# Kernel tuning notes

Measured on AMD Instinct MI355X. Metric: run time of the kernel, lower is better.

Reference implementation:

```python
import jax, jax.numpy as jnp
import numpy as np

N_NODES = 50000


def gcn_conv(x, W, b, src, dst, n_nodes):
    """PyG-style GCNConv: out = D^{-1/2} (A + I) D^{-1/2} (x W) + b."""
    xw = x @ W  # [N, out_dim]
    loop = jnp.arange(n_nodes, dtype=src.dtype)
    src_f = jnp.concatenate([src, loop])  # edges + self-loops
    dst_f = jnp.concatenate([dst, loop])
    deg = jax.ops.segment_sum(jnp.ones_like(dst_f, dtype=xw.dtype), dst_f,
                              num_segments=n_nodes)
    dinv = jnp.where(deg > 0, jax.lax.rsqrt(deg), 0.0)
    norm = dinv[src_f] * dinv[dst_f]  # [E+N]
    msgs = xw[src_f] * norm[:, None]  # gather + scale
    out = jax.ops.segment_sum(msgs, dst_f, num_segments=n_nodes)
    return out + b


def setup_inputs() -> dict:
    key = jax.random.key(0)
    ks = jax.random.split(key, 8)
    n, e = N_NODES, 800000
    in_d, hid, out_d = 128, 256, 64
    x = jax.random.normal(ks[0], (n, in_d), dtype=jnp.float32)
    edge_index = jax.random.randint(ks[1], (2, e), 0, n, dtype=jnp.int32)
    sc = lambda f: 1.0 / np.sqrt(f)
    W1 = jax.random.normal(ks[2], (in_d, hid), dtype=jnp.float32) * sc(in_d)
    b1 = jnp.zeros((hid,), jnp.float32)
    W2 = jax.random.normal(ks[3], (hid, hid), dtype=jnp.float32) * sc(hid)
    b2 = jnp.zeros((hid,), jnp.float32)
    W_final = jax.random.normal(ks[4], (hid, out_d), dtype=jnp.float32) * sc(hid)
    b_final = jnp.zeros((out_d,), jnp.float32)
    W_skip = jax.random.normal(ks[5], (in_d, out_d), dtype=jnp.float32) * sc(in_d)
    b_skip = jnp.zeros((out_d,), jnp.float32)
    return {"x": x, "edge_index": edge_index, "W1": W1, "b1": b1,
            "W2": W2, "b2": b2, "W_final": W_final, "b_final": b_final,
            "W_skip": W_skip, "b_skip": b_skip}


def reference(x, edge_index, W1, b1, W2, b2, W_final, b_final, W_skip, b_skip):
    n = x.shape[0]
    src, dst = edge_index[0], edge_index[1]
    h = jax.nn.relu(gcn_conv(x, W1, b1, src, dst, n))
    h = jax.nn.relu(gcn_conv(h, W2, b2, src, dst, n))
    return h @ W_final + b_final + (x @ W_skip + b_skip)
```

## Files before the change

### kernel.cpp

```cpp
#include <hip/hip_runtime.h>

#define N_NODES 50000
#define N_EDGES 800000
#define HB 782

typedef float f32x4 __attribute__((ext_vector_type(4)));
typedef float f32x2 __attribute__((ext_vector_type(2)));
typedef __bf16 bf16x8 __attribute__((ext_vector_type(8)));
typedef __bf16 bf16x4 __attribute__((ext_vector_type(4)));


__global__ void zero_deg(int4* __restrict__ p, int n4) {
    int i = blockIdx.x * blockDim.x + threadIdx.x;
    if (i < n4) p[i] = make_int4(0, 0, 0, 0);
}

#define CAST_N4 (N_NODES * 32)
#define PREP_ITEMS (CAST_N4 + 32768 + 65536 + 16384 + 8192 + 64)
#define PREP_BLOCKS ((PREP_ITEMS + 255) / 256)

__global__ void mega_prep(const int* __restrict__ dst, int* __restrict__ deg,
                          int* __restrict__ rank,
                          const float* __restrict__ x, __bf16* __restrict__ x_bf,
                          const float* __restrict__ W1, const float* __restrict__ W2,
                          const float* __restrict__ Wf, const float* __restrict__ Ws,
                          const float* __restrict__ bfb, const float* __restrict__ bsb,
                          __bf16* __restrict__ W1t, __bf16* __restrict__ W2t,
                          __bf16* __restrict__ Wft, __bf16* __restrict__ Wst,
                          float* __restrict__ bfinal) {
    int b = blockIdx.x;
    if (b < HB) {
        int i = (b * 256 + threadIdx.x) * 4;
        if (i >= N_EDGES) return;
        int4 d = *(const int4*)(dst + i);
        int4 r;
        r.x = atomicAdd(&deg[d.x], 1);
        r.y = atomicAdd(&deg[d.y], 1);
        r.z = atomicAdd(&deg[d.z], 1);
        r.w = atomicAdd(&deg[d.w], 1);
        *(int4*)(rank + i) = r;
        return;
    }
    int idx = (b - HB) * 256 + threadIdx.x;
    if (idx < CAST_N4) {
        float4 v = ((const float4*)x)[idx];
        bf16x4 a = {(__bf16)v.x, (__bf16)v.y, (__bf16)v.z, (__bf16)v.w};
        __builtin_nontemporal_store(a, (bf16x4*)x_bf + idx);
        return;
    }
    int j = idx - CAST_N4;
    if (j < 32768) {
        int n = j >> 7, k = j & 127;
        W1t[j] = (__bf16)W1[k * 256 + n];
    } else if (j < 32768 + 65536) {
        int i = j - 32768;
        int n = i >> 8, k = i & 255;
        W2t[i] = (__bf16)W2[k * 256 + n];
    } else if (j < 32768 + 65536 + 16384) {
        int i = j - (32768 + 65536);
        int n = i >> 8, k = i & 255;
        Wft[i] = (__bf16)Wf[k * 64 + n];
    } else if (j < 32768 + 65536 + 16384 + 8192) {
        int i = j - (32768 + 65536 + 16384);
        int n = i >> 7, k = i & 127;
        Wst[i] = (__bf16)Ws[k * 64 + n];
    } else if (j < 32768 + 65536 + 16384 + 8192 + 64) {
        int i = j - (32768 + 65536 + 16384 + 8192);
        bfinal[i] = bfb[i] + bsb[i];
    }
}

__device__ __forceinline__ int wave_incl_scan(int x) {
    int lane = threadIdx.x & 63;
#pragma unroll
    for (int off = 1; off < 64; off <<= 1) {
        int y = __shfl_up(x, off, 64);
        if (lane >= off) x += y;
    }
    return x;
}

__global__ void scan_partial_dinv(const int* __restrict__ in, int n,
                                  int* __restrict__ out_partial, int* __restrict__ blocksum,
                                  float* __restrict__ dinv) {
    __shared__ int wsum[8];
    int i = blockIdx.x * 512 + threadIdx.x;
    int v = (i < n) ? in[i] : 0;
    if (i < n) dinv[i] = rsqrtf((float)(v + 1));
    int inc = wave_incl_scan(v);
    int lane = threadIdx.x & 63, wid = threadIdx.x >> 6;
    if (lane == 63) wsum[wid] = inc;
    __syncthreads();
    if (wid == 0) {
        int w = (lane < 8) ? wsum[lane] : 0;
        int wi = wave_incl_scan(w);
        if (lane < 8) wsum[lane] = wi;
    }
    __syncthreads();
    int woff = (wid == 0) ? 0 : wsum[wid - 1];
    if (i < n) out_partial[i] = woff + inc - v;
    if (threadIdx.x == 0) blocksum[blockIdx.x] = wsum[7];
}

#define SCAN_NB 98
#define XS_ITEMS (N_NODES * 16)
#define XS_BLOCKS ((XS_ITEMS + 511) / 512)

__global__ __launch_bounds__(512) void scan_add_xs(int* __restrict__ rowptr, int n,
                                                   const int* __restrict__ blocksum, int nb, int total,
                                                   const __bf16* __restrict__ x_bf,
                                                   const float* __restrict__ dinv,
                                                   unsigned char* __restrict__ x_s8) {
    int b = blockIdx.x;
    if (b < SCAN_NB) {
        __shared__ int sexc[128];
        __shared__ int w0tot;
        int t = threadIdx.x;
        if (t < 128) {
            int v = (t < nb) ? blocksum[t] : 0;
            int inc = wave_incl_scan(v);
            sexc[t] = inc - v;
            if (t == 63) w0tot = inc;
        }
        __syncthreads();
        int boff = sexc[b] + (b >= 64 ? w0tot : 0);
        int i = b * 512 + t;
        if (i < n) rowptr[i] += boff;
        if (i == 0) rowptr[n] = total;
        return;
    }
    int j = (b - SCAN_NB) * 512 + threadIdx.x;
    if (j < XS_ITEMS) {
        bf16x8 v = ((const bf16x8*)x_bf)[j];
        float di = dinv[j >> 4];
        float f[8];
#pragma unroll
        for (int k = 0; k < 8; ++k) f[k] = di * (float)v[k];
        int w0 = __builtin_amdgcn_cvt_pk_fp8_f32(f[0], f[1], 0, false);
        w0 = __builtin_amdgcn_cvt_pk_fp8_f32(f[2], f[3], w0, true);
        int w1 = __builtin_amdgcn_cvt_pk_fp8_f32(f[4], f[5], 0, false);
        w1 = __builtin_amdgcn_cvt_pk_fp8_f32(f[6], f[7], w1, true);
        ((uint2*)x_s8)[j] = make_uint2((unsigned)w0, (unsigned)w1);
    }
}

__global__ void fill_csr(const int* __restrict__ src, const int* __restrict__ dst,
                         const int* __restrict__ rank,
                         const int* __restrict__ rowptr, int* __restrict__ csr_src) {
    int i = (blockIdx.x * blockDim.x + threadIdx.x) * 4;
    if (i >= N_EDGES) return;
    int4 d = *(const int4*)(dst + i);
    int4 s = *(const int4*)(src + i);
    int4 r = *(const int4*)(rank + i);
    csr_src[rowptr[d.x] + r.x] = s.x;
    csr_src[rowptr[d.y] + r.y] = s.y;
    csr_src[rowptr[d.z] + r.z] = s.z;
    csr_src[rowptr[d.w] + r.w] = s.w;
}


template <int F> struct LdSel;
template <> struct LdSel<128> { using T = unsigned int; };
template <> struct LdSel<256> { using T = uint2; };

template <int F>
__global__ __launch_bounds__(256) void aggregate_fp8(const unsigned char* __restrict__ in_s, __bf16* __restrict__ out,
                                                     const int* __restrict__ rowptr, const int* __restrict__ csr_src,
                                                     const float* __restrict__ dinv) {
    constexpr int BPL = F / 32;
    using LT = typename LdSel<F>::T;
    int node = blockIdx.x * 4 + (threadIdx.x >> 6);
    int lane = threadIdx.x & 63;
    int lh = lane & 31;
    int half = lane >> 5;
    const unsigned char* colbase = in_s + lh * BPL;

    float acc[BPL] = {};
    auto decode_acc = [&](LT v) {
        if constexpr (BPL == 4) {
            f32x2 p0 = __builtin_amdgcn_cvt_pk_f32_fp8(v, false);
            f32x2 p1 = __builtin_amdgcn_cvt_pk_f32_fp8(v, true);
            acc[0] += p0[0]; acc[1] += p0[1]; acc[2] += p1[0]; acc[3] += p1[1];
        } else {
            f32x2 p0 = __builtin_amdgcn_cvt_pk_f32_fp8(v.x, false);
            f32x2 p1 = __builtin_amdgcn_cvt_pk_f32_fp8(v.x, true);
            f32x2 p2 = __builtin_amdgcn_cvt_pk_f32_fp8(v.y, false);
            f32x2 p3 = __builtin_amdgcn_cvt_pk_f32_fp8(v.y, true);
            acc[0] += p0[0]; acc[1] += p0[1]; acc[2] += p1[0]; acc[3] += p1[1];
            acc[4] += p2[0]; acc[5] += p2[1]; acc[6] += p3[0]; acc[7] += p3[1];
        }
    };

    if (half == 0) decode_acc(*(const LT*)(colbase + (size_t)node * F));

    int beg = rowptr[node], end = rowptr[node + 1];
    int e = beg;
    for (; e + 16 <= end; e += 16) {
        int ss[8];
#pragma unroll
        for (int k = 0; k < 8; ++k) ss[k] = csr_src[e + 2 * k + half];
        LT v[8];
#pragma unroll
        for (int k = 0; k < 8; ++k) v[k] = *(const LT*)(colbase + (size_t)ss[k] * F);
#pragma unroll
        for (int k = 0; k < 8; ++k) decode_acc(v[k]);
    }
    for (; e + 8 <= end; e += 8) {
        int s0 = csr_src[e + half], s1 = csr_src[e + 2 + half];
        int s2 = csr_src[e + 4 + half], s3 = csr_src[e + 6 + half];
        LT v0 = *(const LT*)(colbase + (size_t)s0 * F);
        LT v1 = *(const LT*)(colbase + (size_t)s1 * F);
        LT v2 = *(const LT*)(colbase + (size_t)s2 * F);
        LT v3 = *(const LT*)(colbase + (size_t)s3 * F);
        decode_acc(v0); decode_acc(v1); decode_acc(v2); decode_acc(v3);
    }
    for (; e + 2 <= end; e += 2) {
        int s = csr_src[e + half];
        decode_acc(*(const LT*)(colbase + (size_t)s * F));
    }
    if (e < end && half == 0) decode_acc(*(const LT*)(colbase + (size_t)csr_src[e] * F));

    float di = dinv[node];
    if constexpr (BPL == 4) {
        bf16x4 o;
#pragma unroll
        for (int j = 0; j < 4; ++j) {
            float t = acc[j] + __shfl_xor(acc[j], 32);
            o[j] = (__bf16)(di * t);
        }
        if (half == 0) __builtin_nontemporal_store(o, (bf16x4*)(out + (size_t)node * F + lh * 4));
    } else {
        bf16x8 o;
#pragma unroll
        for (int j = 0; j < 8; ++j) {
            float t = acc[j] + __shfl_xor(acc[j], 32);
            o[j] = (__bf16)(di * t);
        }
        if (half == 0) __builtin_nontemporal_store(o, (bf16x8*)(out + (size_t)node * F + lh * 8));
    }
}


template <int NROWS, int NTH>
__device__ __forceinline__ void stage_tile(const __bf16* __restrict__ src, int K, int row0, int rowclamp,
                                           int k0, char* lds) {
    int t = threadIdx.x;
#pragma unroll
    for (int p = 0; p < NROWS * 8 / NTH; ++p) {
        int G = p * NTH + t;
        int r = G >> 3, gp = G & 7;
        int g = gp ^ (r & 7);
        int gr = row0 + r;
        if (gr > rowclamp) gr = rowclamp;
        const __bf16* sp = src + (size_t)gr * K + k0 + g * 8;
        __builtin_amdgcn_global_load_lds((const __attribute__((address_space(1))) void*)sp,
                                         (__attribute__((address_space(3))) void*)(lds + G * 16), 16, 0, 0);
    }
}


template <bool SCALE, bool OUT_FP8>
__global__ __launch_bounds__(512, 4) void mfma_gemm_wide(const __bf16* __restrict__ A, const __bf16* __restrict__ Bt,
                                                         int K, const float* __restrict__ bias,
                                                         const float* __restrict__ dinv,
                                                         void* __restrict__ Cout, int M) {
    constexpr int N = 256;
    __shared__ alignas(16) char lds[81920];
    const int lane = threadIdx.x & 63, wid = threadIdx.x >> 6;
    const int row0 = blockIdx.x * 64;
    const int kg = lane >> 4, l15 = lane & 15;

    f32x4 acc[4][2];
#pragma unroll
    for (int mi = 0; mi < 4; ++mi)
#pragma unroll
        for (int ni = 0; ni < 2; ++ni) acc[mi][ni] = {0.f, 0.f, 0.f, 0.f};

    auto STAGE = [&](int buf, int k0) {
        char* base = lds + buf * 40960;
        stage_tile<64, 512>(A, K, row0, M - 1, k0, base);
        stage_tile<256, 512>(Bt, K, 0, N - 1, k0, base + 8192);
    };

    const int nt = K >> 6;
    STAGE(0, 0);
    __syncthreads();
    int cur = 0;
    for (int t = 0; t < nt; ++t) {
        if (t + 1 < nt) STAGE(cur ^ 1, (t + 1) * 64);
        char* As = lds + cur * 40960;
        char* Bs = As + 8192;
        bf16x8 af[4][2], bfr[2][2];
#pragma unroll
        for (int mi = 0; mi < 4; ++mi) {
            int r = mi * 16 + l15;
#pragma unroll
            for (int kf = 0; kf < 2; ++kf) {
                int slot = (kf * 4 + kg) ^ (r & 7);
                af[mi][kf] = *(const bf16x8*)(As + r * 128 + slot * 16);
            }
        }
#pragma unroll
        for (int ni = 0; ni < 2; ++ni) {
            int r = wid * 32 + ni * 16 + l15;
#pragma unroll
            for (int kf = 0; kf < 2; ++kf) {
                int slot = (kf * 4 + kg) ^ (r & 7);
                bfr[ni][kf] = *(const bf16x8*)(Bs + r * 128 + slot * 16);
            }
        }
#pragma unroll
        for (int mi = 0; mi < 4; ++mi)
#pragma unroll
            for (int ni = 0; ni < 2; ++ni)
#pragma unroll
                for (int kf = 0; kf < 2; ++kf)
                    acc[mi][ni] = __builtin_amdgcn_mfma_f32_16x16x32_bf16(af[mi][kf], bfr[ni][kf],
                                                                          acc[mi][ni], 0, 0, 0);
        __syncthreads();
        cur ^= 1;
    }

#pragma unroll
    for (int mi = 0; mi < 4; ++mi) {
#pragma unroll
        for (int q = 0; q < 4; ++q) {
            int gr = row0 + mi * 16 + kg * 4 + q;
            if (gr >= M) continue;
            float sc = SCALE ? dinv[gr] : 1.0f;
            int col0 = wid * 32 + l15;
            float v0 = fmaxf(acc[mi][0][q] + bias[col0], 0.f);
            float v1 = fmaxf(acc[mi][1][q] + bias[col0 + 16], 0.f);
            if (SCALE) { v0 *= sc; v1 *= sc; }
            if constexpr (OUT_FP8) {
                int w = __builtin_amdgcn_cvt_pk_fp8_f32(v0, v1, 0, false);
                unsigned char* Cp = (unsigned char*)Cout + (size_t)gr * N;
                Cp[col0] = (unsigned char)(w & 0xff);
                Cp[col0 + 16] = (unsigned char)((w >> 8) & 0xff);
            } else {
                __bf16* Cp = (__bf16*)Cout + (size_t)gr * N;
                Cp[col0] = (__bf16)v0;
                Cp[col0 + 16] = (__bf16)v1;
            }
        }
    }
}


__global__ __launch_bounds__(256, 4) void mfma_gemm_final(const __bf16* __restrict__ A1, const __bf16* __restrict__ B1t, int K1,
                                                          const __bf16* __restrict__ A2, const __bf16* __restrict__ B2t, int K2,
                                                          const float* __restrict__ bias, float* __restrict__ Cout, int M) {
    constexpr int N = 64;
    __shared__ alignas(16) char lds[32768];
    const int lane = threadIdx.x & 63, wid = threadIdx.x >> 6;
    const int wm = wid >> 1, wn = wid & 1;
    const int row0 = blockIdx.x * 64;
    const int kg = lane >> 4, l15 = lane & 15;

    f32x4 acc[2][2];
#pragma unroll
    for (int mi = 0; mi < 2; ++mi)
#pragma unroll
        for (int ni = 0; ni < 2; ++ni) acc[mi][ni] = {0.f, 0.f, 0.f, 0.f};

    const int nt1 = K1 >> 6, nt = nt1 + (K2 >> 6);
    auto STAGE = [&](int buf, int tile) {
        const __bf16* A = (tile < nt1) ? A1 : A2;
        const __bf16* Bt = (tile < nt1) ? B1t : B2t;
        int K = (tile < nt1) ? K1 : K2;
        int k0 = ((tile < nt1) ? tile : tile - nt1) * 64;
        char* base = lds + buf * 16384;
        stage_tile<64, 256>(A, K, row0, M - 1, k0, base);
        stage_tile<64, 256>(Bt, K, 0, N - 1, k0, base + 8192);
    };

    STAGE(0, 0);
    __syncthreads();
    int cur = 0;
    for (int t = 0; t < nt; ++t) {
        if (t + 1 < nt) STAGE(cur ^ 1, t + 1);
        char* As = lds + cur * 16384;
        char* Bs = As + 8192;
        bf16x8 af[2][2], bfr[2][2];
#pragma unroll
        for (int mi = 0; mi < 2; ++mi) {
            int r = wm * 32 + mi * 16 + l15;
#pragma unroll
            for (int kf = 0; kf < 2; ++kf) {
                int slot = (kf * 4 + kg) ^ (r & 7);
                af[mi][kf] = *(const bf16x8*)(As + r * 128 + slot * 16);
            }
        }
#pragma unroll
        for (int ni = 0; ni < 2; ++ni) {
            int r = wn * 32 + ni * 16 + l15;
#pragma unroll
            for (int kf = 0; kf < 2; ++kf) {
                int slot = (kf * 4 + kg) ^ (r & 7);
                bfr[ni][kf] = *(const bf16x8*)(Bs + r * 128 + slot * 16);
            }
        }
#pragma unroll
        for (int mi = 0; mi < 2; ++mi)
#pragma unroll
            for (int ni = 0; ni < 2; ++ni)
#pragma unroll
                for (int kf = 0; kf < 2; ++kf)
                    acc[mi][ni] = __builtin_amdgcn_mfma_f32_16x16x32_bf16(af[mi][kf], bfr[ni][kf],
                                                                          acc[mi][ni], 0, 0, 0);
        __syncthreads();
        cur ^= 1;
    }

#pragma unroll
    for (int mi = 0; mi < 2; ++mi) {
#pragma unroll
        for (int ni = 0; ni < 2; ++ni) {
            int col = wn * 32 + ni * 16 + l15;
            float bv = bias[col];
#pragma unroll
            for (int q = 0; q < 4; ++q) {
                int gr = row0 + wm * 32 + mi * 16 + kg * 4 + q;
                if (gr < M) Cout[(size_t)gr * N + col] = acc[mi][ni][q] + bv;
            }
        }
    }
}


extern "C" void kernel_launch(void* const* d_in, const int* in_sizes, int n_in,
                              void* d_out, int out_size, void* d_ws, size_t ws_size,
                              hipStream_t stream) {
    const float* x  = (const float*)d_in[0];
    const int*   ei = (const int*)d_in[1];
    const int*   src = ei;
    const int*   dst = ei + N_EDGES;
    const float* W1 = (const float*)d_in[2];
    const float* b1 = (const float*)d_in[3];
    const float* W2 = (const float*)d_in[4];
    const float* b2 = (const float*)d_in[5];
    const float* Wf = (const float*)d_in[6];
    const float* bf = (const float*)d_in[7];
    const float* Ws = (const float*)d_in[8];
    const float* bs = (const float*)d_in[9];
    float* out = (float*)d_out;

    char* ws = (char*)d_ws;
    size_t off = 0;
    auto alloc = [&](size_t bytes) -> void* {
        void* p = ws + off;
        off += (bytes + 255) & ~(size_t)255;
        return p;
    };
    int*           deg      = (int*)alloc(N_NODES * 4);
    int*           rank     = (int*)alloc(N_EDGES * 4);
    int*           rowptr   = (int*)alloc((N_NODES + 1) * 4);
    float*         dinv     = (float*)alloc(N_NODES * 4);
    int*           blocksum = (int*)alloc(4096);
    int*           csr      = (int*)alloc(N_EDGES * 4);
    __bf16*        x_bf     = (__bf16*)alloc((size_t)N_NODES * 128 * 2);
    unsigned char* x_s8     = (unsigned char*)alloc((size_t)N_NODES * 128);
    __bf16*        W1t      = (__bf16*)alloc(128 * 256 * 2);
    __bf16*        W2t      = (__bf16*)alloc(256 * 256 * 2);
    __bf16*        Wft      = (__bf16*)alloc(256 * 64 * 2);
    __bf16*        Wst      = (__bf16*)alloc(128 * 64 * 2);
    float*         bfinal   = (float*)alloc(64 * 4);
    __bf16*        bufP1    = (__bf16*)alloc((size_t)N_NODES * 256 * 2);
    unsigned char* bufP2    = (unsigned char*)alloc((size_t)N_NODES * 256);
    __bf16*        bufP3    = (__bf16*)alloc((size_t)N_NODES * 256 * 2);

    zero_deg<<<(N_NODES / 4 + 255) / 256, 256, 0, stream>>>((int4*)deg, N_NODES / 4);

    mega_prep<<<HB + PREP_BLOCKS, 256, 0, stream>>>(dst, deg, rank, x, x_bf,
                                                    W1, W2, Wf, Ws, bf, bs,
                                                    W1t, W2t, Wft, Wst, bfinal);

    scan_partial_dinv<<<SCAN_NB, 512, 0, stream>>>(deg, N_NODES, rowptr, blocksum, dinv);

    scan_add_xs<<<SCAN_NB + XS_BLOCKS, 512, 0, stream>>>(rowptr, N_NODES, blocksum, SCAN_NB, N_EDGES,
                                                         x_bf, dinv, x_s8);

    fill_csr<<<HB, 256, 0, stream>>>(src, dst, rank, rowptr, csr);

    const int gm64 = (N_NODES + 63) / 64;

    aggregate_fp8<128><<<(N_NODES + 3) / 4, 256, 0, stream>>>(x_s8, bufP1, rowptr, csr, dinv);
    mfma_gemm_wide<true, true><<<gm64, 512, 0, stream>>>(bufP1, W1t, 128, b1, dinv, bufP2, N_NODES);

    aggregate_fp8<256><<<(N_NODES + 3) / 4, 256, 0, stream>>>(bufP2, bufP3, rowptr, csr, dinv);
    mfma_gemm_wide<false, false><<<gm64, 512, 0, stream>>>(bufP3, W2t, 256, b2, nullptr, bufP1, N_NODES);

    mfma_gemm_final<<<gm64, 256, 0, stream>>>(bufP1, Wft, 256, x_bf, Wst, 128, bfinal, out, N_NODES);
}
```

Baseline: 183.9 us.

## Compute skip GEMM alongside CSR fill and accumulate final GEMM into output

Moves the x@W_skip + bias skip-branch GEMM out of the final GEMM into extra blocks of the CSR fill kernel, so it runs concurrently with the memory-bound scatter. The final GEMM then only does the K=256 product and read-modify-writes into the output. This shortens the tail kernel's K loop but adds a read of the fp32 output in the last kernel and LDS usage to the fill kernel.

```diff
diff --git a/kernel.cpp b/kernel.cpp
--- a/kernel.cpp
+++ b/kernel.cpp
@@ -144,18 +144,111 @@
     }
 }
 
-__global__ void fill_csr(const int* __restrict__ src, const int* __restrict__ dst,
-                         const int* __restrict__ rank,
-                         const int* __restrict__ rowptr, int* __restrict__ csr_src) {
-    int i = (blockIdx.x * blockDim.x + threadIdx.x) * 4;
-    if (i >= N_EDGES) return;
-    int4 d = *(const int4*)(dst + i);
-    int4 s = *(const int4*)(src + i);
-    int4 r = *(const int4*)(rank + i);
-    csr_src[rowptr[d.x] + r.x] = s.x;
-    csr_src[rowptr[d.y] + r.y] = s.y;
-    csr_src[rowptr[d.z] + r.z] = s.z;
-    csr_src[rowptr[d.w] + r.w] = s.w;
+
+template <int NROWS, int NTH>
+__device__ __forceinline__ void stage_tile(const __bf16* __restrict__ src, int K, int row0, int rowclamp,
+                                           int k0, char* lds) {
+    int t = threadIdx.x;
+#pragma unroll
+    for (int p = 0; p < NROWS * 8 / NTH; ++p) {
+        int G = p * NTH + t;
+        int r = G >> 3, gp = G & 7;
+        int g = gp ^ (r & 7);
+        int gr = row0 + r;
+        if (gr > rowclamp) gr = rowclamp;
+        const __bf16* sp = src + (size_t)gr * K + k0 + g * 8;
+        __builtin_amdgcn_global_load_lds((const __attribute__((address_space(1))) void*)sp,
+                                         (__attribute__((address_space(3))) void*)(lds + G * 16), 16, 0, 0);
+    }
+}
+
+
+__global__ __launch_bounds__(256) void fill_skip(const int* __restrict__ src, const int* __restrict__ dst,
+                                                 const int* __restrict__ rank, const int* __restrict__ rowptr,
+                                                 int* __restrict__ csr_src,
+                                                 const __bf16* __restrict__ x_bf, const __bf16* __restrict__ Wst,
+                                                 const float* __restrict__ bfinal, float* __restrict__ out) {
+    int b = blockIdx.x;
+    if (b < HB) {
+        int i = (b * 256 + threadIdx.x) * 4;
+        if (i >= N_EDGES) return;
+        int4 d = *(const int4*)(dst + i);
+        int4 s = *(const int4*)(src + i);
+        int4 r = *(const int4*)(rank + i);
+        csr_src[rowptr[d.x] + r.x] = s.x;
+        csr_src[rowptr[d.y] + r.y] = s.y;
+        csr_src[rowptr[d.z] + r.z] = s.z;
+        csr_src[rowptr[d.w] + r.w] = s.w;
+        return;
+    }
+    constexpr int N = 64, K = 128;
+    __shared__ alignas(16) char lds[32768];
+    const int lane = threadIdx.x & 63, wid = threadIdx.x >> 6;
+    const int wm = wid >> 1, wn = wid & 1;
+    const int row0 = (b - HB) * 64;
+    const int kg = lane >> 4, l15 = lane & 15;
+
+    f32x4 acc[2][2];
+#pragma unroll
+    for (int mi = 0; mi < 2; ++mi)
+#pragma unroll
+        for (int ni = 0; ni < 2; ++ni) acc[mi][ni] = {0.f, 0.f, 0.f, 0.f};
+
+    auto STAGE = [&](int buf, int k0) {
+        char* base = lds + buf * 16384;
+        stage_tile<64, 256>(x_bf, K, row0, N_NODES - 1, k0, base);
+        stage_tile<64, 256>(Wst, K, 0, N - 1, k0, base + 8192);
+    };
+    STAGE(0, 0);
+    __syncthreads();
+    int cur = 0;
+    for (int t = 0; t < 2; ++t) {
+        if (t == 0) STAGE(1, 64);
+        char* As = lds + cur * 16384;
+        char* Bs = As + 8192;
+        bf16x8 af[2][2], bfr[2][2];
+#pragma unroll
+        for (int mi = 0; mi < 2; ++mi) {
+            int r = wm * 32 + mi * 16 + l15;
+#pragma unroll
+            for (int kf = 0; kf < 2; ++kf) {
+                int slot = (kf * 4 + kg) ^ (r & 7);
+                af[mi][kf] = *(const bf16x8*)(As + r * 128 + slot * 16);
+            }
+        }
+#pragma unroll
+        for (int ni = 0; ni < 2; ++ni) {
+            int r = wn * 32 + ni * 16 + l15;
+#pragma unroll
+            for (int kf = 0; kf < 2; ++kf) {
+                int slot = (kf * 4 + kg) ^ (r & 7);
+                bfr[ni][kf] = *(const bf16x8*)(Bs + r * 128 + slot * 16);
+            }
+        }
+#pragma unroll
+        for (int mi = 0; mi < 2; ++mi)
+#pragma unroll
+            for (int ni = 0; ni < 2; ++ni)
+#pragma unroll
+                for (int kf = 0; kf < 2; ++kf)
+                    acc[mi][ni] = __builtin_amdgcn_mfma_f32_16x16x32_bf16(af[mi][kf], bfr[ni][kf],
+                                                                          acc[mi][ni], 0, 0, 0);
+        __syncthreads();
+        cur ^= 1;
+    }
+#pragma unroll
+    for (int mi = 0; mi < 2; ++mi) {
+#pragma unroll
+        for (int ni = 0; ni < 2; ++ni) {
+            int col = wn * 32 + ni * 16 + l15;
+            float bv = bfinal[col];
+#pragma unroll
+            for (int q = 0; q < 4; ++q) {
+                int gr = row0 + wm * 32 + mi * 16 + kg * 4 + q;
+                if (gr < N_NODES) out[(size_t)gr * N + col] = acc[mi][ni][q] + bv;
+            }
+        }
+    }
 }
 
 
@@ -237,24 +330,6 @@
             o[j] = (__bf16)(di * t);
         }
         if (half == 0) __builtin_nontemporal_store(o, (bf16x8*)(out + (size_t)node * F + lh * 8));
-    }
-}
-
-
-template <int NROWS, int NTH>
-__device__ __forceinline__ void stage_tile(const __bf16* __restrict__ src, int K, int row0, int rowclamp,
-                                           int k0, char* lds) {
-    int t = threadIdx.x;
-#pragma unroll
-    for (int p = 0; p < NROWS * 8 / NTH; ++p) {
-        int G = p * NTH + t;
-        int r = G >> 3, gp = G & 7;
-        int g = gp ^ (r & 7);
-        int gr = row0 + r;
-        if (gr > rowclamp) gr = rowclamp;
-        const __bf16* sp = src + (size_t)gr * K + k0 + g * 8;
-        __builtin_amdgcn_global_load_lds((const __attribute__((address_space(1))) void*)sp,
-                                         (__attribute__((address_space(3))) void*)(lds + G * 16), 16, 0, 0);
     }
 }
 
@@ -347,9 +422,8 @@
 }
 
 
-__global__ __launch_bounds__(256, 4) void mfma_gemm_final(const __bf16* __restrict__ A1, const __bf16* __restrict__ B1t, int K1,
-                                                          const __bf16* __restrict__ A2, const __bf16* __restrict__ B2t, int K2,
-                                                          const float* __restrict__ bias, float* __restrict__ Cout, int M) {
+__global__ __launch_bounds__(256, 4) void mfma_gemm_accum(const __bf16* __restrict__ A, const __bf16* __restrict__ Bt,
+                                                          int K, float* __restrict__ Cout, int M) {
     constexpr int N = 64;
     __shared__ alignas(16) char lds[32768];
     const int lane = threadIdx.x & 63, wid = threadIdx.x >> 6;
@@ -363,15 +437,11 @@
 #pragma unroll
         for (int ni = 0; ni < 2; ++ni) acc[mi][ni] = {0.f, 0.f, 0.f, 0.f};
 
-    const int nt1 = K1 >> 6, nt = nt1 + (K2 >> 6);
+    const int nt = K >> 6;
     auto STAGE = [&](int buf, int tile) {
-        const __bf16* A = (tile < nt1) ? A1 : A2;
-        const __bf16* Bt = (tile < nt1) ? B1t : B2t;
-        int K = (tile < nt1) ? K1 : K2;
-        int k0 = ((tile < nt1) ? tile : tile - nt1) * 64;
         char* base = lds + buf * 16384;
-        stage_tile<64, 256>(A, K, row0, M - 1, k0, base);
-        stage_tile<64, 256>(Bt, K, 0, N - 1, k0, base + 8192);
+        stage_tile<64, 256>(A, K, row0, M - 1, tile * 64, base);
+        stage_tile<64, 256>(Bt, K, 0, N - 1, tile * 64, base + 8192);
     };
 
     STAGE(0, 0);
@@ -417,11 +487,10 @@
 #pragma unroll
         for (int ni = 0; ni < 2; ++ni) {
             int col = wn * 32 + ni * 16 + l15;
-            float bv = bias[col];
 #pragma unroll
             for (int q = 0; q < 4; ++q) {
                 int gr = row0 + wm * 32 + mi * 16 + kg * 4 + q;
-                if (gr < M) Cout[(size_t)gr * N + col] = acc[mi][ni][q] + bv;
+                if (gr < M) Cout[(size_t)gr * N + col] += acc[mi][ni][q];
             }
         }
     }
@@ -480,9 +549,10 @@
     scan_add_xs<<<SCAN_NB + XS_BLOCKS, 512, 0, stream>>>(rowptr, N_NODES, blocksum, SCAN_NB, N_EDGES,
                                                          x_bf, dinv, x_s8);
 
-    fill_csr<<<HB, 256, 0, stream>>>(src, dst, rank, rowptr, csr);
-
     const int gm64 = (N_NODES + 63) / 64;
+
+    fill_skip<<<HB + gm64, 256, 0, stream>>>(src, dst, rank, rowptr, csr,
+                                             x_bf, Wst, bfinal, out);
 
     aggregate_fp8<128><<<(N_NODES + 3) / 4, 256, 0, stream>>>(x_s8, bufP1, rowptr, csr, dinv);
     mfma_gemm_wide<true, true><<<gm64, 512, 0, stream>>>(bufP1, W1t, 128, b1, dinv, bufP2, N_NODES);
@@ -490,5 +560,5 @@
     aggregate_fp8<256><<<(N_NODES + 3) / 4, 256, 0, stream>>>(bufP2, bufP3, rowptr, csr, dinv);
     mfma_gemm_wide<false, false><<<gm64, 512, 0, stream>>>(bufP3, W2t, 256, b2, nullptr, bufP1, N_NODES);
 
-    mfma_gemm_final<<<gm64, 256, 0, stream>>>(bufP1, Wft, 256, x_bf, Wst, 128, bfinal, out, N_NODES);
-}
+    mfma_gemm_accum<<<gm64, 256, 0, stream>>>(bufP1, Wft, 256, out, N_NODES);
+}
```

Result: slower. 189.8 us (+3.2%).
